# Optimization experiments

Measured on AMD Instinct MI355X. Metric: run time of the kernel, lower is better.

Reference implementation:

```python
import jax, jax.numpy as jnp
import numpy as np

N = 200000      # nodes per graph batch side
E = 3200000     # edges per side (avg degree 16)
NG = 1000       # number of graphs per side
CIN = 64
F1, F2, F3, D = 64, 32, 16, 16
BN_EPS = 1e-5


def gin_conv(x, edge_index, eps, W1, b1, W2, b2, gamma, beta):
    # GINConv: nn((1+eps)*x + sum_{j->i} x_j), nn = Lin-ReLU-Lin-BatchNorm1d (batch stats)
    src, dst = edge_index[0], edge_index[1]
    agg = jax.ops.segment_sum(x[src], dst, num_segments=x.shape[0])
    h = (1.0 + eps) * x + agg
    h = jax.nn.relu(h @ W1 + b1) @ W2 + b2
    mu = jnp.mean(h, axis=0)
    var = jnp.var(h, axis=0)
    return gamma * (h - mu) * jax.lax.rsqrt(var + BN_EPS) + beta


def global_attention_readout(x, batch, W, b):
    # global_mean_pool -> sigmoid fc -> gated global_add_pool
    ones = jnp.ones((x.shape[0], 1), x.dtype)
    cnt = jax.ops.segment_sum(ones, batch, num_segments=NG)
    summ = jax.ops.segment_sum(x, batch, num_segments=NG)
    mean = summ / jnp.maximum(cnt, 1.0)
    c = jax.nn.sigmoid(mean @ W + b)          # [NG, F3]
    c_n = c[batch]                             # broadcast back to nodes
    gate = jax.nn.sigmoid(jnp.sum(x * c_n, axis=1, keepdims=True))
    return jax.ops.segment_sum(gate * x, batch, num_segments=NG)


def efn(h_i, h_j, aW1, ab1, aW2, ab2, mW, mb):
    h = jnp.concatenate([h_i, h_j], axis=1)   # [NG, 2*F3]
    att = jnp.tanh(jax.nn.relu(h @ aW1 + ab1) @ aW2 + ab2)
    enc = att * h + h
    return jax.nn.relu(enc @ mW + mb)         # [NG, D]


def setup_inputs() -> dict:
    key = jax.random.key(0)
    ks = iter(jax.random.split(key, 48))
    def nrm(shape, s=0.1):
        return jax.random.normal(next(ks), shape, jnp.float32) * s
    inp = {}
    inp["x_i"] = jax.random.normal(next(ks), (N, CIN), jnp.float32)
    inp["x_j"] = jax.random.normal(next(ks), (N, CIN), jnp.float32)
    inp["edge_index_i"] = jax.random.randint(next(ks), (2, E), 0, N, dtype=jnp.int32)
    inp["edge_index_j"] = jax.random.randint(next(ks), (2, E), 0, N, dtype=jnp.int32)
    inp["batch_i"] = jnp.sort(jax.random.randint(next(ks), (N,), 0, NG, dtype=jnp.int32))
    inp["batch_j"] = jnp.sort(jax.random.randint(next(ks), (N,), 0, NG, dtype=jnp.int32))
    # GINConv 1 (train_eps=True, init 0)
    inp["eps1"] = jnp.zeros((), jnp.float32)
    inp["g1_W1"], inp["g1_b1"] = nrm((CIN, F1)), jnp.zeros((F1,), jnp.float32)
    inp["g1_W2"], inp["g1_b2"] = nrm((F1, F1)), jnp.zeros((F1,), jnp.float32)
    inp["g1_g"], inp["g1_bt"] = jnp.ones((F1,), jnp.float32), jnp.zeros((F1,), jnp.float32)
    inp["eps2"] = jnp.zeros((), jnp.float32)
    inp["g2_W1"], inp["g2_b1"] = nrm((F1, F2)), jnp.zeros((F2,), jnp.float32)
    inp["g2_W2"], inp["g2_b2"] = nrm((F2, F2)), jnp.zeros((F2,), jnp.float32)
    inp["g2_g"], inp["g2_bt"] = jnp.ones((F2,), jnp.float32), jnp.zeros((F2,), jnp.float32)
    inp["eps3"] = jnp.zeros((), jnp.float32)
    inp["g3_W1"], inp["g3_b1"] = nrm((F2, F3)), jnp.zeros((F3,), jnp.float32)
    inp["g3_W2"], inp["g3_b2"] = nrm((F3, F3)), jnp.zeros((F3,), jnp.float32)
    inp["g3_g"], inp["g3_bt"] = jnp.ones((F3,), jnp.float32), jnp.zeros((F3,), jnp.float32)
    # global attention fc
    inp["att_W"], inp["att_b"] = nrm((F3, F3)), jnp.zeros((F3,), jnp.float32)
    # EFN: in=2*F3=32, reduction=4 -> 8
    inp["efn_aW1"], inp["efn_ab1"] = nrm((2 * F3, 8)), jnp.zeros((8,), jnp.float32)
    inp["efn_aW2"], inp["efn_ab2"] = nrm((8, 2 * F3)), jnp.zeros((2 * F3,), jnp.float32)
    inp["efn_mW"], inp["efn_mb"] = nrm((2 * F3, D)), jnp.zeros((D,), jnp.float32)
    # final fc: D -> D//2 -> 1
    inp["fc_W1"], inp["fc_b1"] = nrm((D, D // 2)), jnp.zeros((D // 2,), jnp.float32)
    inp["fc_W2"], inp["fc_b2"] = nrm((D // 2, 1)), jnp.zeros((1,), jnp.float32)
    return inp


def reference(x_i, x_j, edge_index_i, edge_index_j, batch_i, batch_j,
              eps1, g1_W1, g1_b1, g1_W2, g1_b2, g1_g, g1_bt,
              eps2, g2_W1, g2_b1, g2_W2, g2_b2, g2_g, g2_bt,
              eps3, g3_W1, g3_b1, g3_W2, g3_b2, g3_g, g3_bt,
              att_W, att_b,
              efn_aW1, efn_ab1, efn_aW2, efn_ab2, efn_mW, efn_mb,
              fc_W1, fc_b1, fc_W2, fc_b2):
    xi1 = gin_conv(x_i, edge_index_i, eps1, g1_W1, g1_b1, g1_W2, g1_b2, g1_g, g1_bt)
    xj1 = gin_conv(x_j, edge_index_j, eps1, g1_W1, g1_b1, g1_W2, g1_b2, g1_g, g1_bt)
    xi2 = gin_conv(xi1, edge_index_i, eps2, g2_W1, g2_b1, g2_W2, g2_b2, g2_g, g2_bt)
    xj2 = gin_conv(xj1, edge_index_j, eps2, g2_W1, g2_b1, g2_W2, g2_b2, g2_g, g2_bt)
    xi3 = gin_conv(xi2, edge_index_i, eps3, g3_W1, g3_b1, g3_W2, g3_b2, g3_g, g3_bt)
    xj3 = gin_conv(xj2, edge_index_j, eps3, g3_W1, g3_b1, g3_W2, g3_b2, g3_g, g3_bt)
    h_i = global_attention_readout(xi3, batch_i, att_W, att_b)
    h_j = global_attention_readout(xj3, batch_j, att_W, att_b)
    h_AB = efn(h_i, h_j, efn_aW1, efn_ab1, efn_aW2, efn_ab2, efn_mW, efn_mb)
    h_AA = efn(h_i, h_i, efn_aW1, efn_ab1, efn_aW2, efn_ab2, efn_mW, efn_mb)
    h_BB = efn(h_j, h_j, efn_aW1, efn_ab1, efn_aW2, efn_ab2, efn_mW, efn_mb)
    h_Ab = h_AB - h_BB
    h_aB = h_AB - h_AA
    score = (jax.nn.relu(h_AB @ fc_W1 + fc_b1) @ fc_W2 + fc_b2).squeeze(1)
    return (score, h_Ab, h_aB)
```

## Files before the change

kernel.cpp:

```cpp
#include <hip/hip_runtime.h>
#include <math.h>

#define NGRAPH 1000
#define BKSHIFT 11
#define BKMASK 2047
#define NBK_MAX 128
#define PART_BLOCKS 256
#define LCAP 33792

typedef unsigned short ushort_t;
typedef __attribute__((ext_vector_type(8))) short short8;
typedef __attribute__((ext_vector_type(8))) _Float16 half8;
typedef __attribute__((ext_vector_type(4))) float floatx4;

static __device__ inline ushort_t f2bf(float f) {
  unsigned u = __float_as_uint(f);
  u = (u + 0x7fffu + ((u >> 16) & 1u)) >> 16;
  return (ushort_t)u;
}
static __device__ inline ushort_t f2h_bits(float f) {
  return __builtin_bit_cast(ushort_t, (_Float16)f);
}
static __device__ inline float h2f_bits(ushort_t u) {
  return (float)__builtin_bit_cast(_Float16, u);
}


__global__ __launch_bounds__(1024) void bucket_hist2(const int* __restrict__ dst0,
                                                     const int* __restrict__ dst1, int E,
                                                     int chunk, int* __restrict__ hist, int nbk) {
  const int side = blockIdx.y;
  const int* __restrict__ dst = side ? dst1 : dst0;
  __shared__ int lh[NBK_MAX];
  for (int i = threadIdx.x; i < nbk; i += 1024) lh[i] = 0;
  __syncthreads();
  const int e0 = blockIdx.x * chunk;
  const int e1 = min(E, e0 + chunk);
  for (int e = e0 + threadIdx.x; e < e1; e += 1024) atomicAdd(&lh[dst[e] >> BKSHIFT], 1);
  __syncthreads();
  int* row = hist + ((size_t)side * PART_BLOCKS + blockIdx.x) * nbk;
  for (int i = threadIdx.x; i < nbk; i += 1024) row[i] = lh[i];
}

__global__ __launch_bounds__(PART_BLOCKS) void colscan_par2(int* __restrict__ hist, int nbk,
                                                            int* __restrict__ totals) {
  __shared__ int s[PART_BLOCKS];
  const int side = blockIdx.y;
  int* __restrict__ hist_s = hist + (size_t)side * PART_BLOCKS * nbk;
  int* __restrict__ totals_s = totals + side * nbk;
  const int b = blockIdx.x;
  const int t = threadIdx.x;
  s[t] = hist_s[(size_t)t * nbk + b];
  __syncthreads();
  for (int off = 1; off < PART_BLOCKS; off <<= 1) {
    int u = (t >= off) ? s[t - off] : 0;
    __syncthreads();
    s[t] += u;
    __syncthreads();
  }
  const int exc = (t == 0) ? 0 : s[t - 1];
  hist_s[(size_t)t * nbk + b] = exc;
  if (t == PART_BLOCKS - 1) totals_s[b] = s[PART_BLOCKS - 1];
}

__global__ __launch_bounds__(1024) void scan_small2(const int* __restrict__ in, int n,
                                                    int* __restrict__ out) {
  __shared__ int s[2048];
  const int side = blockIdx.x;
  const int* __restrict__ in_s = in + side * n;
  int* __restrict__ out_s = out + side * (n + 1);
  const int t = threadIdx.x;
  s[t] = (t < n) ? in_s[t] : 0;
  s[t + 1024] = (t + 1024 < n) ? in_s[t + 1024] : 0;
  __syncthreads();
  for (int off = 1; off < 2048; off <<= 1) {
    int v0 = (t >= off) ? s[t - off] : 0;
    int v1 = ((t + 1024) >= off) ? s[t + 1024 - off] : 0;
    __syncthreads();
    s[t] += v0;
    s[t + 1024] += v1;
    __syncthreads();
  }
  if (t < n) out_s[t] = (t == 0) ? 0 : s[t - 1];
  const int u = t + 1024;
  if (u < n) out_s[u] = s[u - 1];
  if (t == 0) out_s[n] = s[n - 1];
}

__global__ __launch_bounds__(1024) void partition2(const int* __restrict__ src0,
                                                   const int* __restrict__ src1,
                                                   const int* __restrict__ dst0,
                                                   const int* __restrict__ dst1, int E, int chunk,
                                                   const int* __restrict__ hist,
                                                   const int* __restrict__ boff,
                                                   unsigned* __restrict__ ebufA,
                                                   unsigned* __restrict__ ebufB, int nbk) {
  const int side = blockIdx.y;
  const int* __restrict__ src = side ? src1 : src0;
  const int* __restrict__ dst = side ? dst1 : dst0;
  const int* __restrict__ boff_s = boff + side * (nbk + 1);
  unsigned* __restrict__ ebuf = side ? ebufB : ebufA;
  __shared__ int lbase[NBK_MAX];
  __shared__ int lcur[NBK_MAX];
  const int* row = hist + ((size_t)side * PART_BLOCKS + blockIdx.x) * nbk;
  for (int i = threadIdx.x; i < nbk; i += 1024) {
    lbase[i] = boff_s[i] + row[i];
    lcur[i] = 0;
  }
  __syncthreads();
  const int e0 = blockIdx.x * chunk;
  const int e1 = min(E, e0 + chunk);
  for (int e = e0 + threadIdx.x; e < e1; e += 1024) {
    int d = dst[e];
    int b = d >> BKSHIFT;
    int pos = lbase[b] + atomicAdd(&lcur[b], 1);
    ebuf[pos] = ((unsigned)src[e] << BKSHIFT) | (unsigned)(d & BKMASK);
  }
}

__global__ __launch_bounds__(1024) void bucket_csr2(const unsigned* __restrict__ ebufA,
                                                    const unsigned* __restrict__ ebufB,
                                                    const int* __restrict__ boff,
                                                    int* __restrict__ row_ptrA,
                                                    int* __restrict__ colA,
                                                    int* __restrict__ row_ptrB,
                                                    int* __restrict__ colB, int N, int E,
                                                    int nbk) {
  __shared__ int cnt[2048];
  __shared__ int lcol[LCAP];
  const int side = blockIdx.y;
  const unsigned* __restrict__ ebuf = side ? ebufB : ebufA;
  const int* __restrict__ boff_s = boff + side * (nbk + 1);
  int* __restrict__ row_ptr = side ? row_ptrB : row_ptrA;
  int* __restrict__ col = side ? colB : colA;
  const int b = blockIdx.x;
  const int node0 = b << BKSHIFT;
  const int nn = min(2048, N - node0);
  const int es = boff_s[b], ee = boff_s[b + 1];
  const int ne = ee - es;
  const int t = threadIdx.x;
  cnt[t] = 0;
  cnt[t + 1024] = 0;
  __syncthreads();
  for (int e = es + t; e < ee; e += 1024) atomicAdd(&cnt[ebuf[e] & (unsigned)BKMASK], 1);
  __syncthreads();
  for (int off = 1; off < 2048; off <<= 1) {
    int v0 = (t >= off) ? cnt[t - off] : 0;
    int v1 = ((t + 1024) >= off) ? cnt[t + 1024 - off] : 0;
    __syncthreads();
    cnt[t] += v0;
    cnt[t + 1024] += v1;
    __syncthreads();
  }
  const int ex0 = (t == 0) ? 0 : cnt[t - 1];
  const int ex1 = cnt[t + 1023];
  if (t < nn) row_ptr[node0 + t] = es + ex0;
  if (t + 1024 < nn) row_ptr[node0 + t + 1024] = es + ex1;
  __syncthreads();
  cnt[t] = ex0;
  cnt[t + 1024] = ex1;
  __syncthreads();
  if (ne <= LCAP) {
    for (int e = es + t; e < ee; e += 1024) {
      unsigned u = ebuf[e];
      int li = (int)(u & (unsigned)BKMASK);
      int pos = atomicAdd(&cnt[li], 1);
      lcol[pos] = (int)(u >> BKSHIFT);
    }
    __syncthreads();
    for (int i = t; i < ne; i += 1024) col[es + i] = lcol[i];
  } else {
    for (int e = es + t; e < ee; e += 1024) {
      unsigned u = ebuf[e];
      int li = (int)(u & (unsigned)BKMASK);
      int pos = es + atomicAdd(&cnt[li], 1);
      col[pos] = (int)(u >> BKSHIFT);
    }
  }
  if (b == 0 && t == 0) row_ptr[N] = E;
}


template <int FIN, int FOUT, bool HAS_BN, bool IN_HALF>
__global__ __launch_bounds__(256) void lin_mfma2(const void* __restrict__ xin0,
                                                 const void* __restrict__ xin1,
                                                 const float* __restrict__ W,
                                                 const float* __restrict__ st0,
                                                 const float* __restrict__ st1,
                                                 const float* __restrict__ gamma,
                                                 const float* __restrict__ beta, float invN,
                                                 ushort_t* __restrict__ y0,
                                                 ushort_t* __restrict__ y1, int n) {
  constexpr int KC = FIN / 32;
  constexpr int FT = FOUT / 16;
  const int side = blockIdx.y;
  const void* __restrict__ xin = side ? xin1 : xin0;
  const float* __restrict__ stats = side ? st1 : st0;
  ushort_t* __restrict__ y = side ? y1 : y0;
  __shared__ _Float16 Whf[FIN * FOUT];
  __shared__ float scv[FIN], ofv[FIN];
  const int tid = threadIdx.x;
  for (int i = tid; i < FIN * FOUT; i += 256) Whf[i] = (_Float16)W[i];
  for (int i = tid; i < FIN; i += 256) {
    if constexpr (HAS_BN) {
      float mu = stats[i] * invN;
      float var = stats[128 + i] * invN - mu * mu;
      float s = gamma[i] * rsqrtf(var + 1e-5f);
      scv[i] = s;
      ofv[i] = beta[i] - s * mu;
    } else {
      scv[i] = 1.f;
      ofv[i] = 0.f;
    }
  }
  __syncthreads();
  const int lane = tid & 63, wv = tid >> 6;
  const int colf = lane & 15, quad = lane >> 4, kbase = quad * 8;

  half8 Bf[FT][KC];
#pragma unroll
  for (int t = 0; t < FT; t++)
#pragma unroll
    for (int c = 0; c < KC; c++)
#pragma unroll
      for (int j = 0; j < 8; j++)
        Bf[t][c][j] = Whf[(c * 32 + kbase + j) * FOUT + t * 16 + colf];

  const floatx4 zero4 = {0.f, 0.f, 0.f, 0.f};
  const int ntiles = (n + 15) >> 4;
  for (int nt = blockIdx.x * 4 + wv; nt < ntiles; nt += gridDim.x * 4) {
    const int node0 = nt << 4;
    const int anode = node0 + colf;
    half8 Af[KC];
#pragma unroll
    for (int c = 0; c < KC; c++) {
      if (anode < n) {
        const int kk = c * 32 + kbase;
        if constexpr (IN_HALF) {
          const ushort_t* hp = (const ushort_t*)xin + (size_t)anode * FIN + kk;
          half8 hv = *(const half8*)hp;
#pragma unroll
          for (int j = 0; j < 8; j++)
            Af[c][j] = (_Float16)fmaf((float)hv[j], scv[kk + j], ofv[kk + j]);
        } else {
          const float* xp = (const float*)xin + (size_t)anode * FIN + kk;
          float4 xa = *(const float4*)xp;
          float4 xb = *(const float4*)(xp + 4);
          Af[c][0] = (_Float16)fmaf(xa.x, scv[kk + 0], ofv[kk + 0]);
          Af[c][1] = (_Float16)fmaf(xa.y, scv[kk + 1], ofv[kk + 1]);
          Af[c][2] = (_Float16)fmaf(xa.z, scv[kk + 2], ofv[kk + 2]);
          Af[c][3] = (_Float16)fmaf(xa.w, scv[kk + 3], ofv[kk + 3]);
          Af[c][4] = (_Float16)fmaf(xb.x, scv[kk + 4], ofv[kk + 4]);
          Af[c][5] = (_Float16)fmaf(xb.y, scv[kk + 5], ofv[kk + 5]);
          Af[c][6] = (_Float16)fmaf(xb.z, scv[kk + 6], ofv[kk + 6]);
          Af[c][7] = (_Float16)fmaf(xb.w, scv[kk + 7], ofv[kk + 7]);
        }
      } else {
        Af[c] = half8{0, 0, 0, 0, 0, 0, 0, 0};
      }
    }
#pragma unroll
    for (int t = 0; t < FT; t++) {
      floatx4 acc = zero4;
#pragma unroll
      for (int c = 0; c < KC; c++)
        acc = __builtin_amdgcn_mfma_f32_16x16x32_f16(Af[c], Bf[t][c], acc, 0, 0, 0);
#pragma unroll
      for (int r = 0; r < 4; r++) {
        const int row = node0 + quad * 4 + r;
        if (row < n) y[(size_t)row * FOUT + t * 16 + colf] = f2bf(acc[r]);
      }
    }
  }
}


template <int F>
__global__ __launch_bounds__(256) void lin2s_mfma2(const ushort_t* __restrict__ m0,
                                                   const ushort_t* __restrict__ m1,
                                                   const float* __restrict__ W,
                                                   const float* __restrict__ b,
                                                   ushort_t* __restrict__ h0,
                                                   ushort_t* __restrict__ h1,
                                                   float* __restrict__ st0,
                                                   float* __restrict__ st1, int n) {
  constexpr int KC = (F + 31) / 32;
  constexpr int FT = F / 16;
  const int side = blockIdx.y;
  const ushort_t* __restrict__ m = side ? m1 : m0;
  ushort_t* __restrict__ h = side ? h1 : h0;
  float* __restrict__ stats = side ? st1 : st0;
  __shared__ ushort_t Wbf[F * F];
  __shared__ float bs[F], ls[F], lsq[F];
  const int tid = threadIdx.x;
  for (int i = tid; i < F * F; i += 256) Wbf[i] = f2bf(W[i]);
  if (tid < F) {
    bs[tid] = b[tid];
    ls[tid] = 0.f;
    lsq[tid] = 0.f;
  }
  __syncthreads();
  const int lane = tid & 63, wv = tid >> 6;
  const int colf = lane & 15, quad = lane >> 4, kbase = quad * 8;

  short8 Bf[FT][KC];
#pragma unroll
  for (int t = 0; t < FT; t++)
#pragma unroll
    for (int c = 0; c < KC; c++)
#pragma unroll
      for (int j = 0; j < 8; j++) {
        const int k = c * 32 + kbase + j;
        Bf[t][c][j] = (k < F) ? (short)Wbf[k * F + t * 16 + colf] : (short)0;
      }

  const floatx4 zero4 = {0.f, 0.f, 0.f, 0.f};
  float ssum[FT], ssq[FT];
#pragma unroll
  for (int t = 0; t < FT; t++) {
    ssum[t] = 0.f;
    ssq[t] = 0.f;
  }

  const int ntiles = (n + 15) >> 4;
  for (int nt = blockIdx.x * 4 + wv; nt < ntiles; nt += gridDim.x * 4) {
    const int node0 = nt << 4;
    const int anode = node0 + colf;
    short8 Af[KC];
#pragma unroll
    for (int c = 0; c < KC; c++) {
      const int kk = c * 32 + kbase;
      if (anode < n && kk < F)
        Af[c] = *(const short8*)(m + (size_t)anode * F + kk);
      else
        Af[c] = short8{0, 0, 0, 0, 0, 0, 0, 0};
    }
#pragma unroll
    for (int t = 0; t < FT; t++) {
      floatx4 acc = zero4;
#pragma unroll
      for (int c = 0; c < KC; c++)
        acc = __builtin_amdgcn_mfma_f32_16x16x32_bf16(Af[c], Bf[t][c], acc, 0, 0, 0);
      const float bv = bs[t * 16 + colf];
#pragma unroll
      for (int r = 0; r < 4; r++) {
        const int row = node0 + quad * 4 + r;
        if (row < n) {
          float o = acc[r] + bv;
          h[(size_t)row * F + t * 16 + colf] = f2h_bits(o);
          ssum[t] += o;
          ssq[t] += o * o;
        }
      }
    }
  }
#pragma unroll
  for (int t = 0; t < FT; t++) {
    atomicAdd(&ls[t * 16 + colf], ssum[t]);
    atomicAdd(&lsq[t * 16 + colf], ssq[t]);
  }
  __syncthreads();
  if (tid < F) {
    atomicAdd(&stats[tid], ls[tid]);
    atomicAdd(&stats[128 + tid], lsq[tid]);
  }
}


template <int F>
__global__ __launch_bounds__(256) void aggrelu_b2(const ushort_t* __restrict__ ya,
                                                  const ushort_t* __restrict__ yb,
                                                  const int* __restrict__ rp0,
                                                  const int* __restrict__ rp1,
                                                  const int* __restrict__ c0,
                                                  const int* __restrict__ c1,
                                                  const float* __restrict__ epsp,
                                                  const float* __restrict__ b1,
                                                  ushort_t* __restrict__ ma,
                                                  ushort_t* __restrict__ mb, int n) {
  constexpr int LPN = F / 8;
  constexpr int NPB = 256 / LPN;
  const int side = blockIdx.y;
  const ushort_t* __restrict__ y = side ? yb : ya;
  const int* __restrict__ row_ptr = side ? rp1 : rp0;
  const int* __restrict__ col = side ? c1 : c0;
  ushort_t* __restrict__ m = side ? mb : ma;
  const int tid = threadIdx.x;
  const int ln = tid / LPN;
  const int fl = tid % LPN;
  const float e1 = 1.0f + epsp[0];
  const float4 b1a = ((const float4*)b1)[fl * 2];
  const float4 b1b = ((const float4*)b1)[fl * 2 + 1];

  const int node = blockIdx.x * NPB + ln;
  if (node >= n) return;
  const uint4* yr = (const uint4*)y;
  const size_t rowi = (size_t)node * LPN + fl;
  const int rs = row_ptr[node], re = row_ptr[node + 1];

  float acc[8];
#pragma unroll
  for (int j = 0; j < 8; j++) acc[j] = 0.f;

  auto addv = [&](uint4 v) {
    acc[0] += __uint_as_float(v.x << 16);
    acc[1] += __uint_as_float(v.x & 0xffff0000u);
    acc[2] += __uint_as_float(v.y << 16);
    acc[3] += __uint_as_float(v.y & 0xffff0000u);
    acc[4] += __uint_as_float(v.z << 16);
    acc[5] += __uint_as_float(v.z & 0xffff0000u);
    acc[6] += __uint_as_float(v.w << 16);
    acc[7] += __uint_as_float(v.w & 0xffff0000u);
  };

  int e = rs;
  for (; e + 8 <= re; e += 8) {
    int d0 = col[e], d1 = col[e + 1], d2 = col[e + 2], d3 = col[e + 3];
    int d4 = col[e + 4], d5 = col[e + 5], d6 = col[e + 6], d7 = col[e + 7];
    uint4 v0 = yr[(size_t)d0 * LPN + fl];
    uint4 v1 = yr[(size_t)d1 * LPN + fl];
    uint4 v2 = yr[(size_t)d2 * LPN + fl];
    uint4 v3 = yr[(size_t)d3 * LPN + fl];
    uint4 v4 = yr[(size_t)d4 * LPN + fl];
    uint4 v5 = yr[(size_t)d5 * LPN + fl];
    uint4 v6 = yr[(size_t)d6 * LPN + fl];
    uint4 v7 = yr[(size_t)d7 * LPN + fl];
    addv(v0);
    addv(v1);
    addv(v2);
    addv(v3);
    addv(v4);
    addv(v5);
    addv(v6);
    addv(v7);
  }
  for (; e + 4 <= re; e += 4) {
    int d0 = col[e], d1 = col[e + 1], d2 = col[e + 2], d3 = col[e + 3];
    uint4 v0 = yr[(size_t)d0 * LPN + fl];
    uint4 v1 = yr[(size_t)d1 * LPN + fl];
    uint4 v2 = yr[(size_t)d2 * LPN + fl];
    uint4 v3 = yr[(size_t)d3 * LPN + fl];
    addv(v0);
    addv(v1);
    addv(v2);
    addv(v3);
  }
  for (; e < re; e++) addv(yr[(size_t)col[e] * LPN + fl]);

  uint4 sv = yr[rowi];
  float r0, r1, r2, r3, r4, r5, r6, r7;
  r0 = fmaxf(fmaf(e1, __uint_as_float(sv.x << 16), acc[0]) + b1a.x, 0.f);
  r1 = fmaxf(fmaf(e1, __uint_as_float(sv.x & 0xffff0000u), acc[1]) + b1a.y, 0.f);
  r2 = fmaxf(fmaf(e1, __uint_as_float(sv.y << 16), acc[2]) + b1a.z, 0.f);
  r3 = fmaxf(fmaf(e1, __uint_as_float(sv.y & 0xffff0000u), acc[3]) + b1a.w, 0.f);
  r4 = fmaxf(fmaf(e1, __uint_as_float(sv.z << 16), acc[4]) + b1b.x, 0.f);
  r5 = fmaxf(fmaf(e1, __uint_as_float(sv.z & 0xffff0000u), acc[5]) + b1b.y, 0.f);
  r6 = fmaxf(fmaf(e1, __uint_as_float(sv.w << 16), acc[6]) + b1b.z, 0.f);
  r7 = fmaxf(fmaf(e1, __uint_as_float(sv.w & 0xffff0000u), acc[7]) + b1b.w, 0.f);
  uint4 o;
  o.x = (unsigned)f2bf(r0) | ((unsigned)f2bf(r1) << 16);
  o.y = (unsigned)f2bf(r2) | ((unsigned)f2bf(r3) << 16);
  o.z = (unsigned)f2bf(r4) | ((unsigned)f2bf(r5) << 16);
  o.w = (unsigned)f2bf(r6) | ((unsigned)f2bf(r7) << 16);
  ((uint4*)m)[rowi] = o;
}


__global__ __launch_bounds__(256) void readout_fused2(
    const ushort_t* __restrict__ h3a, const ushort_t* __restrict__ h3b,
    const int* __restrict__ batch0, const int* __restrict__ batch1, int n,
    const float* __restrict__ st0, const float* __restrict__ st1,
    const float* __restrict__ gamma, const float* __restrict__ beta, float invN,
    const float* __restrict__ attW, const float* __restrict__ attb,
    float* __restrict__ hgA, float* __restrict__ hgB, int ng) {
  __shared__ float sM[16], oM[16], red[16][17], meanM[16], cM[16];
  __shared__ int seg[2];
  const int side = blockIdx.y;
  const ushort_t* __restrict__ h3 = side ? h3b : h3a;
  const int* __restrict__ batch = side ? batch1 : batch0;
  const float* __restrict__ stats = side ? st1 : st0;
  float* __restrict__ hg = side ? hgB : hgA;
  const int tid = threadIdx.x;
  const int g = blockIdx.x;
  const int f = tid & 15, slot = tid >> 4;
  if (tid < 16) {
    float mu = stats[tid] * invN;
    float var = stats[128 + tid] * invN - mu * mu;
    float s = gamma[tid] * rsqrtf(var + 1e-5f);
    sM[tid] = s;
    oM[tid] = beta[tid] - s * mu;
  }
  if (tid >= 32 && tid < 34) {
    const int key = g + (tid - 32);
    int lo = 0, hi = n;
    while (lo < hi) {
      int mid = (lo + hi) >> 1;
      if (batch[mid] < key) lo = mid + 1; else hi = mid;
    }
    seg[tid - 32] = lo;
  }
  __syncthreads();
  const int s0 = seg[0], e0 = seg[1];
  const float sf = sM[f], of = oM[f];

  float acc = 0.f;
  for (int node = s0 + slot; node < e0; node += 16)
    acc += fmaf(h2f_bits(h3[(size_t)node * 16 + f]), sf, of);
  red[slot][f] = acc;
  __syncthreads();
  if (tid < 16) {
    float t = 0.f;
    for (int s = 0; s < 16; s++) t += red[s][tid];
    meanM[tid] = t / fmaxf((float)(e0 - s0), 1.f);
  }
  __syncthreads();
  if (tid < 16) {
    float a = attb[tid];
    for (int k = 0; k < 16; k++) a += meanM[k] * attW[k * 16 + tid];
    cM[tid] = 1.f / (1.f + expf(-a));
  }
  __syncthreads();
  const float cf = cM[f];
  float acc2 = 0.f;
  for (int node = s0 + slot; node < e0; node += 16) {
    float xv = fmaf(h2f_bits(h3[(size_t)node * 16 + f]), sf, of);
    float p = xv * cf;
    for (int m = 8; m >= 1; m >>= 1) p += __shfl_xor(p, m, 16);
    acc2 += xv / (1.f + expf(-p));
  }
  red[slot][f] = acc2;
  __syncthreads();
  if (tid < 16) {
    float t = 0.f;
    for (int s = 0; s < 16; s++) t += red[s][tid];
    hg[g * 16 + tid] = t;
  }
}


__global__ __launch_bounds__(256) void final3_kernel(
    const float* __restrict__ hgA, const float* __restrict__ hgB, const float* __restrict__ aW1,
    const float* __restrict__ ab1, const float* __restrict__ aW2, const float* __restrict__ ab2,
    const float* __restrict__ mW, const float* __restrict__ mb, const float* __restrict__ fcW1,
    const float* __restrict__ fcb1, const float* __restrict__ fcW2,
    const float* __restrict__ fcb2, float* __restrict__ out, int ng) {
  __shared__ float aW1s[256], aW2s[256], mWs[512], fcW1s[128];
  __shared__ float ab1s[8], ab2s[32], mbs[16], fcb1s[8], fcW2s[8];
  __shared__ float fcb2s;
  __shared__ float hb[16][33], m8b[16][9], encb[16][33], abb[16][17], tb[16][9];
  const int tid = threadIdx.x;
  aW1s[tid] = aW1[tid];
  aW2s[tid] = aW2[tid];
  mWs[tid] = mW[tid];
  mWs[256 + tid] = mW[256 + tid];
  if (tid < 128) fcW1s[tid] = fcW1[tid];
  if (tid < 8) {
    ab1s[tid] = ab1[tid];
    fcb1s[tid] = fcb1[tid];
    fcW2s[tid] = fcW2[tid];
  }
  if (tid < 32) ab2s[tid] = ab2[tid];
  if (tid < 16) mbs[tid] = mb[tid];
  if (tid == 0) fcb2s = fcb2[0];
  __syncthreads();

  const int g = tid >> 4;
  const int l = tid & 15;
  const int gg = blockIdx.x * 16 + g;
  const bool valid = gg < ng;
  const float hiv = valid ? hgA[gg * 16 + l] : 0.f;
  const float hjv = valid ? hgB[gg * 16 + l] : 0.f;
  float res[3];

#pragma unroll
  for (int p = 0; p < 3; p++) {
    float ha = (p == 2) ? hjv : hiv;
    float h2 = (p == 1) ? hiv : hjv;
    hb[g][l] = ha;
    hb[g][16 + l] = h2;
    __syncthreads();
    if (l < 8) {
      float t = ab1s[l];
#pragma unroll
      for (int k = 0; k < 32; k++) t += hb[g][k] * aW1s[k * 8 + l];
      m8b[g][l] = fmaxf(t, 0.f);
    }
    __syncthreads();
    float e0 = ab2s[l], e1 = ab2s[16 + l];
#pragma unroll
    for (int k = 0; k < 8; k++) {
      float mv = m8b[g][k];
      e0 += mv * aW2s[k * 32 + l];
      e1 += mv * aW2s[k * 32 + 16 + l];
    }
    float a0 = tanhf(e0), a1 = tanhf(e1);
    encb[g][l] = fmaf(a0, ha, ha);
    encb[g][16 + l] = fmaf(a1, h2, h2);
    __syncthreads();
    float o = mbs[l];
#pragma unroll
    for (int k = 0; k < 32; k++) o += encb[g][k] * mWs[k * 16 + l];
    res[p] = fmaxf(o, 0.f);
    __syncthreads();
  }

  if (valid) {
    out[ng + gg * 16 + l] = res[0] - res[2];
    out[ng + ng * 16 + gg * 16 + l] = res[0] - res[1];
  }
  abb[g][l] = res[0];
  __syncthreads();
  if (l < 8) {
    float t = fcb1s[l];
#pragma unroll
    for (int k = 0; k < 16; k++) t += abb[g][k] * fcW1s[k * 8 + l];
    tb[g][l] = fmaxf(t, 0.f);
  }
  __syncthreads();
  if (l == 0 && valid) {
    float sc = fcb2s;
#pragma unroll
    for (int o = 0; o < 8; o++) sc += tb[g][o] * fcW2s[o];
    out[gg] = sc;
  }
}


extern "C" void kernel_launch(void* const* d_in, const int* in_sizes, int n_in, void* d_out,
                              int out_size, void* d_ws, size_t ws_size, hipStream_t stream) {
  (void)n_in;
  (void)out_size;
  (void)ws_size;
  const int N = in_sizes[0] / 64;
  const int E = in_sizes[2] / 2;
  const int NG = NGRAPH;
  const int NBK = (N + BKMASK) >> BKSHIFT;
  const int CHUNK = (E + PART_BLOCKS - 1) / PART_BLOCKS;

  char* w = (char*)d_ws;
  auto alloc = [&](size_t bytes) -> void* {
    void* p = (void*)w;
    w += (bytes + 255) & ~(size_t)255;
    return p;
  };
  int* row_ptrA = (int*)alloc((size_t)(N + 1) * 4);
  int* colA = (int*)alloc((size_t)E * 4);
  int* row_ptrB = (int*)alloc((size_t)(N + 1) * 4);
  int* colB = (int*)alloc((size_t)E * 4);
  int* hist = (int*)alloc((size_t)2 * PART_BLOCKS * NBK * 4);
  int* totals = (int*)alloc((size_t)2 * NBK * 4);
  int* boff = (int*)alloc((size_t)2 * (NBK + 1) * 4);
  ushort_t* sA = (ushort_t*)alloc((size_t)2 * N * 64 * 2);
  ushort_t* sB = (ushort_t*)alloc((size_t)2 * N * 64 * 2);
  float* stats = (float*)alloc((size_t)2 * 768 * 4);
  float* hgA = (float*)alloc((size_t)NG * 16 * 4);
  float* hgB = (float*)alloc((size_t)NG * 16 * 4);

  ushort_t* bA[2] = {sA, sA + (size_t)N * 64};
  ushort_t* bB[2] = {sB, sB + (size_t)N * 64};
  unsigned* ebuf0 = (unsigned*)bA[0];
  unsigned* ebuf1 = (unsigned*)bA[1];

  const int* esrc0 = (const int*)d_in[2];
  const int* edst0 = esrc0 + E;
  const int* esrc1 = (const int*)d_in[3];
  const int* edst1 = esrc1 + E;
  const int* batch0 = (const int*)d_in[4];
  const int* batch1 = (const int*)d_in[5];
  const float* attW = (const float*)d_in[27];
  const float* attb = (const float*)d_in[28];
  const float invN = 1.0f / (float)N;

  bucket_hist2<<<dim3(PART_BLOCKS, 2), 1024, 0, stream>>>(edst0, edst1, E, CHUNK, hist, NBK);
  colscan_par2<<<dim3(NBK, 2), PART_BLOCKS, 0, stream>>>(hist, NBK, totals);
  scan_small2<<<2, 1024, 0, stream>>>(totals, NBK, boff);
  partition2<<<dim3(PART_BLOCKS, 2), 1024, 0, stream>>>(esrc0, esrc1, edst0, edst1, E, CHUNK,
                                                        hist, boff, ebuf0, ebuf1, NBK);
  bucket_csr2<<<dim3(NBK, 2), 1024, 0, stream>>>(ebuf0, ebuf1, boff, row_ptrA, colA, row_ptrB,
                                                 colB, N, E, NBK);
  hipMemsetAsync(stats, 0, 2 * 768 * 4, stream);

  float* st0 = stats;
  float* st1 = stats + 768;

  lin_mfma2<64, 64, false, false><<<dim3(512, 2), 256, 0, stream>>>(
      d_in[0], d_in[1], (const float*)d_in[7], nullptr, nullptr, nullptr, nullptr, invN,
      bB[0], bB[1], N);
  aggrelu_b2<64><<<dim3((N + 31) / 32, 2), 256, 0, stream>>>(
      bB[0], bB[1], row_ptrA, row_ptrB, colA, colB, (const float*)d_in[6],
      (const float*)d_in[8], bA[0], bA[1], N);
  lin2s_mfma2<64><<<dim3(512, 2), 256, 0, stream>>>(bA[0], bA[1], (const float*)d_in[9],
                                                    (const float*)d_in[10], bB[0], bB[1],
                                                    st0, st1, N);

  lin_mfma2<64, 32, true, true><<<dim3(512, 2), 256, 0, stream>>>(
      bB[0], bB[1], (const float*)d_in[14], st0, st1, (const float*)d_in[11],
      (const float*)d_in[12], invN, bA[0], bA[1], N);
  aggrelu_b2<32><<<dim3((N + 63) / 64, 2), 256, 0, stream>>>(
      bA[0], bA[1], row_ptrA, row_ptrB, colA, colB, (const float*)d_in[13],
      (const float*)d_in[15], bA[0] + (size_t)N * 32, bA[1] + (size_t)N * 32, N);
  lin2s_mfma2<32><<<dim3(512, 2), 256, 0, stream>>>(
      bA[0] + (size_t)N * 32, bA[1] + (size_t)N * 32, (const float*)d_in[16],
      (const float*)d_in[17], bB[0], bB[1], st0 + 256, st1 + 256, N);

  lin_mfma2<32, 16, true, true><<<dim3(512, 2), 256, 0, stream>>>(
      bB[0], bB[1], (const float*)d_in[21], st0 + 256, st1 + 256, (const float*)d_in[18],
      (const float*)d_in[19], invN, bA[0], bA[1], N);
  aggrelu_b2<16><<<dim3((N + 127) / 128, 2), 256, 0, stream>>>(
      bA[0], bA[1], row_ptrA, row_ptrB, colA, colB, (const float*)d_in[20],
      (const float*)d_in[22], bA[0] + (size_t)N * 16, bA[1] + (size_t)N * 16, N);
  lin2s_mfma2<16><<<dim3(512, 2), 256, 0, stream>>>(
      bA[0] + (size_t)N * 16, bA[1] + (size_t)N * 16, (const float*)d_in[23],
      (const float*)d_in[24], bB[0], bB[1], st0 + 512, st1 + 512, N);

  readout_fused2<<<dim3(NG, 2), 256, 0, stream>>>(
      bB[0], bB[1], batch0, batch1, N, st0 + 512, st1 + 512, (const float*)d_in[25],
      (const float*)d_in[26], invN, attW, attb, hgA, hgB, NG);

  final3_kernel<<<(NG + 15) / 16, 256, 0, stream>>>(
      hgA, hgB, (const float*)d_in[29], (const float*)d_in[30], (const float*)d_in[31],
      (const float*)d_in[32], (const float*)d_in[33], (const float*)d_in[34],
      (const float*)d_in[35], (const float*)d_in[36], (const float*)d_in[37],
      (const float*)d_in[38], (float*)d_out, NG);
}
```

Before: 738.3 us.

## Fuse neighbor aggregation+ReLU with second linear layer via LDS staging

Merges the aggregation/ReLU kernel with the second MFMA linear plus batch-stat kernel for each GIN layer. Aggregated rows are written to shared memory and consumed there by the MFMA matmul, so the intermediate activation no longer makes a round trip through global memory and one launch per layer goes away. In exchange, each small block now loads and converts the weight matrix into LDS and does a block-level stats reduction, and B fragments are re-read from LDS per tile. Buffer ping-pong assignments are adjusted to match.

```diff
diff --git a/kernel.cpp b/kernel.cpp
--- a/kernel.cpp
+++ b/kernel.cpp
@@ -276,44 +276,126 @@
 
 
 template <int F>
-__global__ __launch_bounds__(256) void lin2s_mfma2(const ushort_t* __restrict__ m0,
-                                                   const ushort_t* __restrict__ m1,
-                                                   const float* __restrict__ W,
-                                                   const float* __restrict__ b,
-                                                   ushort_t* __restrict__ h0,
-                                                   ushort_t* __restrict__ h1,
-                                                   float* __restrict__ st0,
-                                                   float* __restrict__ st1, int n) {
+__global__ __launch_bounds__(256) void agg_lin2f(const ushort_t* __restrict__ ya,
+                                                 const ushort_t* __restrict__ yb,
+                                                 const int* __restrict__ rp0,
+                                                 const int* __restrict__ rp1,
+                                                 const int* __restrict__ c0,
+                                                 const int* __restrict__ c1,
+                                                 const float* __restrict__ epsp,
+                                                 const float* __restrict__ b1,
+                                                 const float* __restrict__ W,
+                                                 const float* __restrict__ b2,
+                                                 ushort_t* __restrict__ h0,
+                                                 ushort_t* __restrict__ h1,
+                                                 float* __restrict__ st0,
+                                                 float* __restrict__ st1, int n) {
+  constexpr int LPN = F / 8;
+  constexpr int NPB = 256 / LPN;
   constexpr int KC = (F + 31) / 32;
   constexpr int FT = F / 16;
+  constexpr int T = NPB / 16;
+  constexpr int TPW = (T + 3) / 4;
+  constexpr int RS = F + 8;
   const int side = blockIdx.y;
-  const ushort_t* __restrict__ m = side ? m1 : m0;
+  const ushort_t* __restrict__ y = side ? yb : ya;
+  const int* __restrict__ row_ptr = side ? rp1 : rp0;
+  const int* __restrict__ col = side ? c1 : c0;
   ushort_t* __restrict__ h = side ? h1 : h0;
   float* __restrict__ stats = side ? st1 : st0;
+
   __shared__ ushort_t Wbf[F * F];
+  __shared__ ushort_t lm[NPB * RS];
   __shared__ float bs[F], ls[F], lsq[F];
   const int tid = threadIdx.x;
   for (int i = tid; i < F * F; i += 256) Wbf[i] = f2bf(W[i]);
   if (tid < F) {
-    bs[tid] = b[tid];
+    bs[tid] = b2[tid];
     ls[tid] = 0.f;
     lsq[tid] = 0.f;
   }
-  __syncthreads();
+
+  const int ln = tid / LPN;
+  const int fl = tid % LPN;
+  const float e1 = 1.0f + epsp[0];
+  const int node = blockIdx.x * NPB + ln;
+  if (node < n) {
+    const float4 b1a = ((const float4*)b1)[fl * 2];
+    const float4 b1b = ((const float4*)b1)[fl * 2 + 1];
+    const uint4* yr = (const uint4*)y;
+    const size_t rowi = (size_t)node * LPN + fl;
+    const int rs = row_ptr[node], re = row_ptr[node + 1];
+
+    float acc[8];
+#pragma unroll
+    for (int j = 0; j < 8; j++) acc[j] = 0.f;
+
+    auto addv = [&](uint4 v) {
+      acc[0] += __uint_as_float(v.x << 16);
+      acc[1] += __uint_as_float(v.x & 0xffff0000u);
+      acc[2] += __uint_as_float(v.y << 16);
+      acc[3] += __uint_as_float(v.y & 0xffff0000u);
+      acc[4] += __uint_as_float(v.z << 16);
+      acc[5] += __uint_as_float(v.z & 0xffff0000u);
+      acc[6] += __uint_as_float(v.w << 16);
+      acc[7] += __uint_as_float(v.w & 0xffff0000u);
+    };
+
+    int e = rs;
+    for (; e + 8 <= re; e += 8) {
+      int d0 = col[e], d1 = col[e + 1], d2 = col[e + 2], d3 = col[e + 3];
+      int d4 = col[e + 4], d5 = col[e + 5], d6 = col[e + 6], d7 = col[e + 7];
+      uint4 v0 = yr[(size_t)d0 * LPN + fl];
+      uint4 v1 = yr[(size_t)d1 * LPN + fl];
+      uint4 v2 = yr[(size_t)d2 * LPN + fl];
+      uint4 v3 = yr[(size_t)d3 * LPN + fl];
+      uint4 v4 = yr[(size_t)d4 * LPN + fl];
+      uint4 v5 = yr[(size_t)d5 * LPN + fl];
+      uint4 v6 = yr[(size_t)d6 * LPN + fl];
+      uint4 v7 = yr[(size_t)d7 * LPN + fl];
+      addv(v0);
+      addv(v1);
+      addv(v2);
+      addv(v3);
+      addv(v4);
+      addv(v5);
+      addv(v6);
+      addv(v7);
+    }
+    for (; e + 4 <= re; e += 4) {
+      int d0 = col[e], d1 = col[e + 1], d2 = col[e + 2], d3 = col[e + 3];
+      uint4 v0 = yr[(size_t)d0 * LPN + fl];
+      uint4 v1 = yr[(size_t)d1 * LPN + fl];
+      uint4 v2 = yr[(size_t)d2 * LPN + fl];
+      uint4 v3 = yr[(size_t)d3 * LPN + fl];
+      addv(v0);
+      addv(v1);
+      addv(v2);
+      addv(v3);
+    }
+    for (; e < re; e++) addv(yr[(size_t)col[e] * LPN + fl]);
+
+    uint4 sv = yr[rowi];
+    float r0, r1, r2, r3, r4, r5, r6, r7;
+    r0 = fmaxf(fmaf(e1, __uint_as_float(sv.x << 16), acc[0]) + b1a.x, 0.f);
+    r1 = fmaxf(fmaf(e1, __uint_as_float(sv.x & 0xffff0000u), acc[1]) + b1a.y, 0.f);
+    r2 = fmaxf(fmaf(e1, __uint_as_float(sv.y << 16), acc[2]) + b1a.z, 0.f);
+    r3 = fmaxf(fmaf(e1, __uint_as_float(sv.y & 0xffff0000u), acc[3]) + b1a.w, 0.f);
+    r4 = fmaxf(fmaf(e1, __uint_as_float(sv.z << 16), acc[4]) + b1b.x, 0.f);
+    r5 = fmaxf(fmaf(e1, __uint_as_float(sv.z & 0xffff0000u), acc[5]) + b1b.y, 0.f);
+    r6 = fmaxf(fmaf(e1, __uint_as_float(sv.w << 16), acc[6]) + b1b.z, 0.f);
+    r7 = fmaxf(fmaf(e1, __uint_as_float(sv.w & 0xffff0000u), acc[7]) + b1b.w, 0.f);
+    uint4 o;
+    o.x = (unsigned)f2bf(r0) | ((unsigned)f2bf(r1) << 16);
+    o.y = (unsigned)f2bf(r2) | ((unsigned)f2bf(r3) << 16);
+    o.z = (unsigned)f2bf(r4) | ((unsigned)f2bf(r5) << 16);
+    o.w = (unsigned)f2bf(r6) | ((unsigned)f2bf(r7) << 16);
+    *(uint4*)&lm[ln * RS + fl * 8] = o;
+  }
+  __syncthreads();
+
   const int lane = tid & 63, wv = tid >> 6;
   const int colf = lane & 15, quad = lane >> 4, kbase = quad * 8;
-
-  short8 Bf[FT][KC];
-#pragma unroll
-  for (int t = 0; t < FT; t++)
-#pragma unroll
-    for (int c = 0; c < KC; c++)
-#pragma unroll
-      for (int j = 0; j < 8; j++) {
-        const int k = c * 32 + kbase + j;
-        Bf[t][c][j] = (k < F) ? (short)Wbf[k * F + t * 16 + colf] : (short)0;
-      }
-
   const floatx4 zero4 = {0.f, 0.f, 0.f, 0.f};
   float ssum[FT], ssq[FT];
 #pragma unroll
@@ -322,34 +404,44 @@
     ssq[t] = 0.f;
   }
 
-  const int ntiles = (n + 15) >> 4;
-  for (int nt = blockIdx.x * 4 + wv; nt < ntiles; nt += gridDim.x * 4) {
-    const int node0 = nt << 4;
-    const int anode = node0 + colf;
-    short8 Af[KC];
-#pragma unroll
-    for (int c = 0; c < KC; c++) {
-      const int kk = c * 32 + kbase;
-      if (anode < n && kk < F)
-        Af[c] = *(const short8*)(m + (size_t)anode * F + kk);
-      else
-        Af[c] = short8{0, 0, 0, 0, 0, 0, 0, 0};
-    }
-#pragma unroll
-    for (int t = 0; t < FT; t++) {
-      floatx4 acc = zero4;
-#pragma unroll
-      for (int c = 0; c < KC; c++)
-        acc = __builtin_amdgcn_mfma_f32_16x16x32_bf16(Af[c], Bf[t][c], acc, 0, 0, 0);
-      const float bv = bs[t * 16 + colf];
-#pragma unroll
-      for (int r = 0; r < 4; r++) {
-        const int row = node0 + quad * 4 + r;
-        if (row < n) {
-          float o = acc[r] + bv;
-          h[(size_t)row * F + t * 16 + colf] = f2h_bits(o);
-          ssum[t] += o;
-          ssq[t] += o * o;
+#pragma unroll
+  for (int tt = 0; tt < TPW; tt++) {
+    const int tile = wv * TPW + tt;
+    if (tile < T) {
+      const int nodeL0 = tile * 16;
+      const int nodeG0 = blockIdx.x * NPB + nodeL0;
+      short8 Af[KC];
+#pragma unroll
+      for (int c = 0; c < KC; c++) {
+        const int kk = c * 32 + kbase;
+        if (nodeG0 + colf < n && kk < F)
+          Af[c] = *(const short8*)&lm[(nodeL0 + colf) * RS + kk];
+        else
+          Af[c] = short8{0, 0, 0, 0, 0, 0, 0, 0};
+      }
+#pragma unroll
+      for (int t = 0; t < FT; t++) {
+        floatx4 acc = zero4;
+#pragma unroll
+        for (int c = 0; c < KC; c++) {
+          short8 Bfr;
+#pragma unroll
+          for (int j = 0; j < 8; j++) {
+            const int k = c * 32 + kbase + j;
+            Bfr[j] = (k < F) ? (short)Wbf[k * F + t * 16 + colf] : (short)0;
+          }
+          acc = __builtin_amdgcn_mfma_f32_16x16x32_bf16(Af[c], Bfr, acc, 0, 0, 0);
+        }
+        const float bv = bs[t * 16 + colf];
+#pragma unroll
+        for (int r = 0; r < 4; r++) {
+          const int row = nodeG0 + quad * 4 + r;
+          if (row < n) {
+            float o = acc[r] + bv;
+            h[(size_t)row * F + t * 16 + colf] = f2h_bits(o);
+            ssum[t] += o;
+            ssq[t] += o * o;
+          }
         }
       }
     }
@@ -364,105 +456,6 @@
     atomicAdd(&stats[tid], ls[tid]);
     atomicAdd(&stats[128 + tid], lsq[tid]);
   }
-}
-
-
-template <int F>
-__global__ __launch_bounds__(256) void aggrelu_b2(const ushort_t* __restrict__ ya,
-                                                  const ushort_t* __restrict__ yb,
-                                                  const int* __restrict__ rp0,
-                                                  const int* __restrict__ rp1,
-                                                  const int* __restrict__ c0,
-                                                  const int* __restrict__ c1,
-                                                  const float* __restrict__ epsp,
-                                                  const float* __restrict__ b1,
-                                                  ushort_t* __restrict__ ma,
-                                                  ushort_t* __restrict__ mb, int n) {
-  constexpr int LPN = F / 8;
-  constexpr int NPB = 256 / LPN;
-  const int side = blockIdx.y;
-  const ushort_t* __restrict__ y = side ? yb : ya;
-  const int* __restrict__ row_ptr = side ? rp1 : rp0;
-  const int* __restrict__ col = side ? c1 : c0;
-  ushort_t* __restrict__ m = side ? mb : ma;
-  const int tid = threadIdx.x;
-  const int ln = tid / LPN;
-  const int fl = tid % LPN;
-  const float e1 = 1.0f + epsp[0];
-  const float4 b1a = ((const float4*)b1)[fl * 2];
-  const float4 b1b = ((const float4*)b1)[fl * 2 + 1];
-
-  const int node = blockIdx.x * NPB + ln;
-  if (node >= n) return;
-  const uint4* yr = (const uint4*)y;
-  const size_t rowi = (size_t)node * LPN + fl;
-  const int rs = row_ptr[node], re = row_ptr[node + 1];
-
-  float acc[8];
-#pragma unroll
-  for (int j = 0; j < 8; j++) acc[j] = 0.f;
-
-  auto addv = [&](uint4 v) {
-    acc[0] += __uint_as_float(v.x << 16);
-    acc[1] += __uint_as_float(v.x & 0xffff0000u);
-    acc[2] += __uint_as_float(v.y << 16);
-    acc[3] += __uint_as_float(v.y & 0xffff0000u);
-    acc[4] += __uint_as_float(v.z << 16);
-    acc[5] += __uint_as_float(v.z & 0xffff0000u);
-    acc[6] += __uint_as_float(v.w << 16);
-    acc[7] += __uint_as_float(v.w & 0xffff0000u);
-  };
-
-  int e = rs;
-  for (; e + 8 <= re; e += 8) {
-    int d0 = col[e], d1 = col[e + 1], d2 = col[e + 2], d3 = col[e + 3];
-    int d4 = col[e + 4], d5 = col[e + 5], d6 = col[e + 6], d7 = col[e + 7];
-    uint4 v0 = yr[(size_t)d0 * LPN + fl];
-    uint4 v1 = yr[(size_t)d1 * LPN + fl];
-    uint4 v2 = yr[(size_t)d2 * LPN + fl];
-    uint4 v3 = yr[(size_t)d3 * LPN + fl];
-    uint4 v4 = yr[(size_t)d4 * LPN + fl];
-    uint4 v5 = yr[(size_t)d5 * LPN + fl];
-    uint4 v6 = yr[(size_t)d6 * LPN + fl];
-    uint4 v7 = yr[(size_t)d7 * LPN + fl];
-    addv(v0);
-    addv(v1);
-    addv(v2);
-    addv(v3);
-    addv(v4);
-    addv(v5);
-    addv(v6);
-    addv(v7);
-  }
-  for (; e + 4 <= re; e += 4) {
-    int d0 = col[e], d1 = col[e + 1], d2 = col[e + 2], d3 = col[e + 3];
-    uint4 v0 = yr[(size_t)d0 * LPN + fl];
-    uint4 v1 = yr[(size_t)d1 * LPN + fl];
-    uint4 v2 = yr[(size_t)d2 * LPN + fl];
-    uint4 v3 = yr[(size_t)d3 * LPN + fl];
-    addv(v0);
-    addv(v1);
-    addv(v2);
-    addv(v3);
-  }
-  for (; e < re; e++) addv(yr[(size_t)col[e] * LPN + fl]);
-
-  uint4 sv = yr[rowi];
-  float r0, r1, r2, r3, r4, r5, r6, r7;
-  r0 = fmaxf(fmaf(e1, __uint_as_float(sv.x << 16), acc[0]) + b1a.x, 0.f);
-  r1 = fmaxf(fmaf(e1, __uint_as_float(sv.x & 0xffff0000u), acc[1]) + b1a.y, 0.f);
-  r2 = fmaxf(fmaf(e1, __uint_as_float(sv.y << 16), acc[2]) + b1a.z, 0.f);
-  r3 = fmaxf(fmaf(e1, __uint_as_float(sv.y & 0xffff0000u), acc[3]) + b1a.w, 0.f);
-  r4 = fmaxf(fmaf(e1, __uint_as_float(sv.z << 16), acc[4]) + b1b.x, 0.f);
-  r5 = fmaxf(fmaf(e1, __uint_as_float(sv.z & 0xffff0000u), acc[5]) + b1b.y, 0.f);
-  r6 = fmaxf(fmaf(e1, __uint_as_float(sv.w << 16), acc[6]) + b1b.z, 0.f);
-  r7 = fmaxf(fmaf(e1, __uint_as_float(sv.w & 0xffff0000u), acc[7]) + b1b.w, 0.f);
-  uint4 o;
-  o.x = (unsigned)f2bf(r0) | ((unsigned)f2bf(r1) << 16);
-  o.y = (unsigned)f2bf(r2) | ((unsigned)f2bf(r3) << 16);
-  o.z = (unsigned)f2bf(r4) | ((unsigned)f2bf(r5) << 16);
-  o.w = (unsigned)f2bf(r6) | ((unsigned)f2bf(r7) << 16);
-  ((uint4*)m)[rowi] = o;
 }
 
 
@@ -686,35 +679,29 @@
   lin_mfma2<64, 64, false, false><<<dim3(512, 2), 256, 0, stream>>>(
       d_in[0], d_in[1], (const float*)d_in[7], nullptr, nullptr, nullptr, nullptr, invN,
       bB[0], bB[1], N);
-  aggrelu_b2<64><<<dim3((N + 31) / 32, 2), 256, 0, stream>>>(
+  agg_lin2f<64><<<dim3((N + 31) / 32, 2), 256, 0, stream>>>(
       bB[0], bB[1], row_ptrA, row_ptrB, colA, colB, (const float*)d_in[6],
-      (const float*)d_in[8], bA[0], bA[1], N);
-  lin2s_mfma2<64><<<dim3(512, 2), 256, 0, stream>>>(bA[0], bA[1], (const float*)d_in[9],
-                                                    (const float*)d_in[10], bB[0], bB[1],
-                                                    st0, st1, N);
+      (const float*)d_in[8], (const float*)d_in[9], (const float*)d_in[10], bA[0], bA[1],
+      st0, st1, N);
 
   lin_mfma2<64, 32, true, true><<<dim3(512, 2), 256, 0, stream>>>(
-      bB[0], bB[1], (const float*)d_in[14], st0, st1, (const float*)d_in[11],
-      (const float*)d_in[12], invN, bA[0], bA[1], N);
-  aggrelu_b2<32><<<dim3((N + 63) / 64, 2), 256, 0, stream>>>(
-      bA[0], bA[1], row_ptrA, row_ptrB, colA, colB, (const float*)d_in[13],
-      (const float*)d_in[15], bA[0] + (size_t)N * 32, bA[1] + (size_t)N * 32, N);
-  lin2s_mfma2<32><<<dim3(512, 2), 256, 0, stream>>>(
-      bA[0] + (size_t)N * 32, bA[1] + (size_t)N * 32, (const float*)d_in[16],
-      (const float*)d_in[17], bB[0], bB[1], st0 + 256, st1 + 256, N);
+      bA[0], bA[1], (const float*)d_in[14], st0, st1, (const float*)d_in[11],
+      (const float*)d_in[12], invN, bB[0], bB[1], N);
+  agg_lin2f<32><<<dim3((N + 63) / 64, 2), 256, 0, stream>>>(
+      bB[0], bB[1], row_ptrA, row_ptrB, colA, colB, (const float*)d_in[13],
+      (const float*)d_in[15], (const float*)d_in[16], (const float*)d_in[17], bA[0], bA[1],
+      st0 + 256, st1 + 256, N);
 
   lin_mfma2<32, 16, true, true><<<dim3(512, 2), 256, 0, stream>>>(
-      bB[0], bB[1], (const float*)d_in[21], st0 + 256, st1 + 256, (const float*)d_in[18],
-      (const float*)d_in[19], invN, bA[0], bA[1], N);
-  aggrelu_b2<16><<<dim3((N + 127) / 128, 2), 256, 0, stream>>>(
-      bA[0], bA[1], row_ptrA, row_ptrB, colA, colB, (const float*)d_in[20],
-      (const float*)d_in[22], bA[0] + (size_t)N * 16, bA[1] + (size_t)N * 16, N);
-  lin2s_mfma2<16><<<dim3(512, 2), 256, 0, stream>>>(
-      bA[0] + (size_t)N * 16, bA[1] + (size_t)N * 16, (const float*)d_in[23],
-      (const float*)d_in[24], bB[0], bB[1], st0 + 512, st1 + 512, N);
+      bA[0], bA[1], (const float*)d_in[21], st0 + 256, st1 + 256, (const float*)d_in[18],
+      (const float*)d_in[19], invN, bB[0], bB[1], N);
+  agg_lin2f<16><<<dim3((N + 127) / 128, 2), 256, 0, stream>>>(
+      bB[0], bB[1], row_ptrA, row_ptrB, colA, colB, (const float*)d_in[20],
+      (const float*)d_in[22], (const float*)d_in[23], (const float*)d_in[24], bA[0], bA[1],
+      st0 + 512, st1 + 512, N);
 
   readout_fused2<<<dim3(NG, 2), 256, 0, stream>>>(
-      bB[0], bB[1], batch0, batch1, N, st0 + 512, st1 + 512, (const float*)d_in[25],
+      bA[0], bA[1], batch0, batch1, N, st0 + 512, st1 + 512, (const float*)d_in[25],
       (const float*)d_in[26], invN, attW, attb, hgA, hgB, NG);
 
   final3_kernel<<<(NG + 15) / 16, 256, 0, stream>>>(
```

Measured after the change: 1.066 ms. 44.4% more time.
